# Kernel optimization log

Measured on AMD Instinct MI355X. Metric: run time of the kernel, lower is better.

## Reference

```python
import jax, jax.numpy as jnp
import numpy as np

N_NODES = 100000

def _mean_aggregate(h, edge_index, num_nodes):
    # PyG convention: edge_index[0]=source j, edge_index[1]=target i; mean over in-neighbors
    src, dst = edge_index[0], edge_index[1]
    summed = jax.ops.segment_sum(h[src], dst, num_segments=num_nodes)  # [N, D]
    cnt = jax.ops.segment_sum(jnp.ones((src.shape[0],), h.dtype), dst, num_segments=num_nodes)
    return summed / jnp.maximum(cnt, 1.0)[:, None]

def _sage_conv(h, edge_index, Wl, bl, Wr, num_nodes):
    agg = _mean_aggregate(h, edge_index, num_nodes)
    return agg @ Wl.T + bl + h @ Wr.T

def setup_inputs() -> dict:
    key = jax.random.key(0)
    ks = jax.random.split(key, 12)
    D = 64
    scale = 1.0 / np.sqrt(D)
    x = jax.random.normal(ks[0], (N_NODES, D), jnp.float32)
    edge_index = jax.random.randint(ks[1], (2, 1000000), 0, N_NODES, jnp.int32)
    edge_label_index = jax.random.randint(ks[2], (2, 200000), 0, N_NODES, jnp.int32)
    def w(k):
        return (jax.random.normal(k, (D, D), jnp.float32) * scale)
    return {
        'x': x,
        'edge_index': edge_index,
        'edge_label_index': edge_label_index,
        'W_lin': w(ks[3]), 'b_lin': jnp.zeros((D,), jnp.float32),
        'Wl1': w(ks[4]), 'bl1': jnp.zeros((D,), jnp.float32), 'Wr1': w(ks[5]),
        'Wl2': w(ks[6]), 'bl2': jnp.zeros((D,), jnp.float32), 'Wr2': w(ks[7]),
    }

def reference(x, edge_index, edge_label_index, W_lin, b_lin, Wl1, bl1, Wr1, Wl2, bl2, Wr2):
    h = x @ W_lin.T + b_lin                                   # node_lin
    h = jax.nn.relu(_sage_conv(h, edge_index, Wl1, bl1, Wr1, N_NODES))  # conv1 + relu
    h = _sage_conv(h, edge_index, Wl2, bl2, Wr2, N_NODES)               # conv2
    # edge dot-product classifier
    preds = jnp.sum(h[edge_label_index[0]] * h[edge_label_index[1]], axis=-1)  # [E_label]
    return preds
```

## Files before the change

### kernel.cpp

```cpp
#include <hip/hip_runtime.h>

#define DD 64
#define BW 256
#define NBMAX 512
#define CAPB 4096
#define CHUNK 8192
#define FILLPAD 16

typedef unsigned short u16;
typedef unsigned char u8;
typedef u16 ushort8v __attribute__((ext_vector_type(8)));
typedef short s16x8 __attribute__((ext_vector_type(8)));
typedef float f32x4 __attribute__((ext_vector_type(4)));
typedef float f32x2 __attribute__((ext_vector_type(2)));

__device__ __forceinline__ float bf2f(u16 u) {
    union { unsigned u32; float f; } x; x.u32 = (unsigned)u << 16; return x.f;
}
__device__ __forceinline__ u16 f2bf(float f) {
    union { float f; unsigned u; } x; x.f = f;
    unsigned r = (x.u + 0x7fffu + ((x.u >> 16) & 1u)) >> 16;
    return (u16)r;
}

__device__ __forceinline__ uint4 pack16_fp8(ushort8v s0, ushort8v s1) {
    uint4 pk;
    int w;
    w = __builtin_amdgcn_cvt_pk_fp8_f32(bf2f(s0[0]), bf2f(s0[1]), 0, false);
    w = __builtin_amdgcn_cvt_pk_fp8_f32(bf2f(s0[2]), bf2f(s0[3]), w, true);
    pk.x = (unsigned)w;
    w = __builtin_amdgcn_cvt_pk_fp8_f32(bf2f(s0[4]), bf2f(s0[5]), 0, false);
    w = __builtin_amdgcn_cvt_pk_fp8_f32(bf2f(s0[6]), bf2f(s0[7]), w, true);
    pk.y = (unsigned)w;
    w = __builtin_amdgcn_cvt_pk_fp8_f32(bf2f(s1[0]), bf2f(s1[1]), 0, false);
    w = __builtin_amdgcn_cvt_pk_fp8_f32(bf2f(s1[2]), bf2f(s1[3]), w, true);
    pk.z = (unsigned)w;
    w = __builtin_amdgcn_cvt_pk_fp8_f32(bf2f(s1[4]), bf2f(s1[5]), 0, false);
    w = __builtin_amdgcn_cvt_pk_fp8_f32(bf2f(s1[6]), bf2f(s1[7]), w, true);
    pk.w = (unsigned)w;
    return pk;
}

#define ACC16(u) do { \
    f32x2 _p; \
    _p = __builtin_amdgcn_cvt_pk_f32_fp8((int)(u).x, false); a[0]  += _p[0]; a[1]  += _p[1]; \
    _p = __builtin_amdgcn_cvt_pk_f32_fp8((int)(u).x, true);  a[2]  += _p[0]; a[3]  += _p[1]; \
    _p = __builtin_amdgcn_cvt_pk_f32_fp8((int)(u).y, false); a[4]  += _p[0]; a[5]  += _p[1]; \
    _p = __builtin_amdgcn_cvt_pk_f32_fp8((int)(u).y, true);  a[6]  += _p[0]; a[7]  += _p[1]; \
    _p = __builtin_amdgcn_cvt_pk_f32_fp8((int)(u).z, false); a[8]  += _p[0]; a[9]  += _p[1]; \
    _p = __builtin_amdgcn_cvt_pk_f32_fp8((int)(u).z, true);  a[10] += _p[0]; a[11] += _p[1]; \
    _p = __builtin_amdgcn_cvt_pk_f32_fp8((int)(u).w, false); a[12] += _p[0]; a[13] += _p[1]; \
    _p = __builtin_amdgcn_cvt_pk_f32_fp8((int)(u).w, true);  a[14] += _p[0]; a[15] += _p[1]; \
} while (0)

__global__ __launch_bounds__(256) void k_partlin(
    const int* __restrict__ ei, int n_edges, int nb_chunk,
    int* __restrict__ fill, unsigned* __restrict__ part,
    const float* __restrict__ w1, const float* __restrict__ w2,
    const float* __restrict__ w3, const float* __restrict__ w4,
    u16* __restrict__ wb,
    const float* __restrict__ A, const float* __restrict__ W,
    const float* __restrict__ bias, u16* __restrict__ out, u8* __restrict__ out8,
    int n_nodes) {
    __shared__ int hist[NBMAX];
    __shared__ int curs[NBMAX];
    __shared__ u16 stage[64 * DD];
    int t = threadIdx.x;
    if ((int)blockIdx.x < nb_chunk) {
        {
            int i = blockIdx.x * 256 + t;
            if (i < 4 * DD * DD) {
                int mat = i >> 12, off = i & 4095;
                const float* src = (mat == 0) ? w1 : (mat == 1) ? w2 : (mat == 2) ? w3 : w4;
                wb[DD * DD + i] = f2bf(src[off]);
            }
        }
        hist[t] = 0; hist[256 + t] = 0;
        __syncthreads();
        int c0 = blockIdx.x * CHUNK;
        int c1 = min(n_edges, c0 + CHUNK);
        int nloc = c1 - c0;
        int nvec = ((n_edges & 3) == 0) ? (nloc & ~3) : 0;
        for (int e4 = t * 4; e4 < nvec; e4 += 1024) {
            int4 d4 = *(const int4*)(ei + n_edges + c0 + e4);
            atomicAdd(&hist[d4.x >> 8], 1);
            atomicAdd(&hist[d4.y >> 8], 1);
            atomicAdd(&hist[d4.z >> 8], 1);
            atomicAdd(&hist[d4.w >> 8], 1);
        }
        for (int e = nvec + t; e < nloc; e += 256)
            atomicAdd(&hist[ei[n_edges + c0 + e] >> 8], 1);
        __syncthreads();
        #pragma unroll
        for (int k = 0; k < 2; ++k) {
            int idx = k * 256 + t;
            int h = hist[idx];
            int base = 0;
            if (h > 0) base = atomicAdd(&fill[idx * FILLPAD], h);
            curs[idx] = base;
        }
        __syncthreads();
        for (int e4 = t * 4; e4 < nvec; e4 += 1024) {
            int4 d4 = *(const int4*)(ei + n_edges + c0 + e4);
            int4 s4 = *(const int4*)(ei + c0 + e4);
            {
                int b = d4.x >> 8; int pos = atomicAdd(&curs[b], 1);
                if (pos < CAPB) part[(size_t)b * CAPB + pos] = ((unsigned)s4.x << 8) | (unsigned)(d4.x & 255);
            }
            {
                int b = d4.y >> 8; int pos = atomicAdd(&curs[b], 1);
                if (pos < CAPB) part[(size_t)b * CAPB + pos] = ((unsigned)s4.y << 8) | (unsigned)(d4.y & 255);
            }
            {
                int b = d4.z >> 8; int pos = atomicAdd(&curs[b], 1);
                if (pos < CAPB) part[(size_t)b * CAPB + pos] = ((unsigned)s4.z << 8) | (unsigned)(d4.z & 255);
            }
            {
                int b = d4.w >> 8; int pos = atomicAdd(&curs[b], 1);
                if (pos < CAPB) part[(size_t)b * CAPB + pos] = ((unsigned)s4.w << 8) | (unsigned)(d4.w & 255);
            }
        }
        for (int e = nvec + t; e < nloc; e += 256) {
            int dst = ei[n_edges + c0 + e];
            int src = ei[c0 + e];
            int b = dst >> 8;
            int pos = atomicAdd(&curs[b], 1);
            if (pos < CAPB)
                part[(size_t)b * CAPB + pos] = ((unsigned)src << 8) | (unsigned)(dst & 255);
        }
    } else {
        int bid = (int)blockIdx.x - nb_chunk;
        int w = t >> 6;
        int lane = t & 63;
        int col = lane & 15;
        int quad = lane >> 4;
        int m0 = bid * 64 + w * 16;
        int arow = m0 + col;
        if (arow > n_nodes - 1) arow = n_nodes - 1;

        f32x4 acc[4];
        #pragma unroll
        for (int nt = 0; nt < 4; ++nt) {
            float bv = bias[nt * 16 + col];
            acc[nt] = (f32x4){bv, bv, bv, bv};
        }
        #pragma unroll
        for (int ks = 0; ks < 2; ++ks) {
            int k0 = ks * 32 + quad * 8;
            const float* p = A + (size_t)arow * DD + k0;
            float4 v0 = *(const float4*)p;
            float4 v1 = *(const float4*)(p + 4);
            s16x8 a;
            a[0] = (short)f2bf(v0.x); a[1] = (short)f2bf(v0.y);
            a[2] = (short)f2bf(v0.z); a[3] = (short)f2bf(v0.w);
            a[4] = (short)f2bf(v1.x); a[5] = (short)f2bf(v1.y);
            a[6] = (short)f2bf(v1.z); a[7] = (short)f2bf(v1.w);
            #pragma unroll
            for (int nt = 0; nt < 4; ++nt) {
                const float* wp = W + (size_t)(nt * 16 + col) * DD + k0;
                float4 b0 = *(const float4*)wp;
                float4 b1 = *(const float4*)(wp + 4);
                s16x8 bfr;
                bfr[0] = (short)f2bf(b0.x); bfr[1] = (short)f2bf(b0.y);
                bfr[2] = (short)f2bf(b0.z); bfr[3] = (short)f2bf(b0.w);
                bfr[4] = (short)f2bf(b1.x); bfr[5] = (short)f2bf(b1.y);
                bfr[6] = (short)f2bf(b1.z); bfr[7] = (short)f2bf(b1.w);
                acc[nt] = __builtin_amdgcn_mfma_f32_16x16x32_bf16(a, bfr, acc[nt], 0, 0, 0);
            }
        }
        #pragma unroll
        for (int nt = 0; nt < 4; ++nt)
            #pragma unroll
            for (int i = 0; i < 4; ++i) {
                int rloc = w * 16 + quad * 4 + i;
                int dsw = (nt * 16 + col) ^ ((rloc & 3) << 4);
                stage[rloc * DD + dsw] = f2bf(acc[nt][i]);
            }
        __threadfence_block();
        {
            int rr = w * 16 + (lane >> 2);
            int sg = lane & 3;
            int m = bid * 64 + rr;
            if (m < n_nodes) {
                int se = (sg ^ (rr & 3)) * 16;
                ushort8v s0 = *(ushort8v*)(stage + rr * DD + se);
                ushort8v s1 = *(ushort8v*)(stage + rr * DD + se + 8);
                *(ushort8v*)(out + (size_t)m * DD + sg * 16) = s0;
                *(ushort8v*)(out + (size_t)m * DD + sg * 16 + 8) = s1;
                *(uint4*)(out8 + (size_t)m * DD + sg * 16) = pack16_fp8(s0, s1);
            }
        }
    }
}

__global__ __launch_bounds__(256) void k_build(const unsigned* __restrict__ part,
                        const int* __restrict__ fill,
                        int* __restrict__ row_start, int* __restrict__ row_deg,
                        int* __restrict__ csr, int n_nodes) {
    __shared__ int cnt_l[BW];
    __shared__ int sc[BW];
    __shared__ unsigned csr_l[CAPB];
    int t = threadIdx.x;
    int b = blockIdx.x;
    int beg = b * CAPB;
    int size = min(fill[b * FILLPAD], CAPB);

    cnt_l[t] = 0;
    __syncthreads();
    for (int j = t; j < size; j += 256)
        atomicAdd(&cnt_l[part[beg + j] & 255], 1);
    __syncthreads();
    int v0 = cnt_l[t];
    sc[t] = v0;
    cnt_l[t] = 0;
    __syncthreads();
    for (int off = 1; off < 256; off <<= 1) {
        int a = (t >= off) ? sc[t - off] : 0;
        __syncthreads();
        if (t >= off) sc[t] += a;
        __syncthreads();
    }
    {
        int n0 = b * BW + t;
        if (n0 < n_nodes) {
            row_start[n0] = beg + ((t == 0) ? 0 : sc[t - 1]);
            row_deg[n0] = v0;
        }
    }
    for (int j = t; j < size; j += 256) {
        unsigned p = part[beg + j];
        int dl = (int)(p & 255u);
        int pos = ((dl == 0) ? 0 : sc[dl - 1]) + atomicAdd(&cnt_l[dl], 1);
        csr_l[pos] = p >> 8;
    }
    __syncthreads();
    for (int i = t; i < size; i += 256) csr[beg + i] = (int)csr_l[i];
}

__global__ __launch_bounds__(256) void k_conv(
    const u16* __restrict__ h, const u8* __restrict__ h8,
    const int* __restrict__ row_start, const int* __restrict__ row_deg,
    const int* __restrict__ csr,
    const u16* __restrict__ Wl, const u16* __restrict__ Wr,
    const float* __restrict__ bias, u16* __restrict__ out, u8* __restrict__ out8,
    int n_nodes, int relu) {
    __shared__ u16 mean_l[64 * DD];
    int t = threadIdx.x;
    int w = t >> 6, lane = t & 63;
    int nn = lane >> 2;
    int r = lane & 3;
    int m0 = blockIdx.x * 64;

    {
        int li = w * 16 + nn;
        int n = m0 + li;
        int beg = 0, end = 0;
        if (n < n_nodes) { beg = row_start[n]; end = beg + row_deg[n]; }
        float a[16];
        #pragma unroll
        for (int kk = 0; kk < 16; ++kk) a[kk] = 0.f;
        int j = beg;
        for (; j + 3 < end; j += 4) {
            int s0 = csr[j], s1 = csr[j + 1], s2 = csr[j + 2], s3 = csr[j + 3];
            uint4 u0 = *(const uint4*)(h8 + (size_t)s0 * DD + r * 16);
            uint4 u1 = *(const uint4*)(h8 + (size_t)s1 * DD + r * 16);
            uint4 u2 = *(const uint4*)(h8 + (size_t)s2 * DD + r * 16);
            uint4 u3 = *(const uint4*)(h8 + (size_t)s3 * DD + r * 16);
            ACC16(u0); ACC16(u1); ACC16(u2); ACC16(u3);
        }
        for (; j < end; ++j) {
            uint4 u0 = *(const uint4*)(h8 + (size_t)csr[j] * DD + r * 16);
            ACC16(u0);
        }
        int deg = end - beg;
        float inv = (deg > 0) ? 1.0f / (float)deg : 0.0f;
        ushort8v o0, o1;
        #pragma unroll
        for (int kk = 0; kk < 8; ++kk) { o0[kk] = f2bf(a[kk] * inv); o1[kk] = f2bf(a[8 + kk] * inv); }
        *(ushort8v*)(mean_l + li * DD + r * 16) = o0;
        *(ushort8v*)(mean_l + li * DD + r * 16 + 8) = o1;
    }
    __threadfence_block();

    int col = lane & 15;
    int quad = lane >> 4;
    int arow = m0 + w * 16 + col;
    if (arow > n_nodes - 1) arow = n_nodes - 1;

    f32x4 acc[4];
    #pragma unroll
    for (int nt = 0; nt < 4; ++nt) {
        float bv = bias[nt * 16 + col];
        acc[nt] = (f32x4){bv, bv, bv, bv};
    }
    #pragma unroll
    for (int ks = 0; ks < 2; ++ks) {
        int k0 = ks * 32 + quad * 8;
        s16x8 am = *(const s16x8*)(mean_l + (w * 16 + col) * DD + k0);
        s16x8 ah = *(const s16x8*)(h + (size_t)arow * DD + k0);
        #pragma unroll
        for (int nt = 0; nt < 4; ++nt) {
            s16x8 bl = *(const s16x8*)(Wl + (nt * 16 + col) * DD + k0);
            acc[nt] = __builtin_amdgcn_mfma_f32_16x16x32_bf16(am, bl, acc[nt], 0, 0, 0);
            s16x8 br = *(const s16x8*)(Wr + (nt * 16 + col) * DD + k0);
            acc[nt] = __builtin_amdgcn_mfma_f32_16x16x32_bf16(ah, br, acc[nt], 0, 0, 0);
        }
    }
    #pragma unroll
    for (int nt = 0; nt < 4; ++nt)
        #pragma unroll
        for (int i = 0; i < 4; ++i) {
            float v = acc[nt][i];
            if (relu) v = fmaxf(v, 0.f);
            int rloc = w * 16 + quad * 4 + i;
            int dsw = (nt * 16 + col) ^ ((rloc & 3) << 4);
            mean_l[rloc * DD + dsw] = f2bf(v);
        }
    __threadfence_block();
    {
        int rr = w * 16 + (lane >> 2);
        int sg = lane & 3;
        int m = m0 + rr;
        if (m < n_nodes) {
            int se = (sg ^ (rr & 3)) * 16;
            ushort8v s0 = *(ushort8v*)(mean_l + rr * DD + se);
            ushort8v s1 = *(ushort8v*)(mean_l + rr * DD + se + 8);
            *(ushort8v*)(out + (size_t)m * DD + sg * 16) = s0;
            *(ushort8v*)(out + (size_t)m * DD + sg * 16 + 8) = s1;
            if (out8)
                *(uint4*)(out8 + (size_t)m * DD + sg * 16) = pack16_fp8(s0, s1);
        }
    }
}

__global__ void k_pred(const u16* __restrict__ h, const int* __restrict__ eli,
                       int n_label, float* __restrict__ out) {
    int t = threadIdx.x;
    int e = blockIdx.x * 16 + (t >> 4);
    if (e >= n_label) return;
    int g = (t >> 3) & 1;
    int r = t & 7;
    int node = g ? eli[n_label + e] : eli[e];
    ushort8v v = *(const ushort8v*)(h + (size_t)node * DD + r * 8);
    float s = 0.f;
    #pragma unroll
    for (int kk = 0; kk < 8; ++kk) {
        float f = bf2f(v[kk]);
        s += f * __shfl_xor(f, 8, 64);
    }
    #pragma unroll
    for (int off = 1; off < 8; off <<= 1) s += __shfl_xor(s, off, 64);
    if ((t & 15) == 0) out[e] = s;
}

extern "C" void kernel_launch(void* const* d_in, const int* in_sizes, int n_in,
                              void* d_out, int out_size, void* d_ws, size_t ws_size,
                              hipStream_t stream) {
    const float* x     = (const float*)d_in[0];
    const int*   ei    = (const int*)d_in[1];
    const int*   eli   = (const int*)d_in[2];
    const float* W_lin = (const float*)d_in[3];
    const float* b_lin = (const float*)d_in[4];
    const float* Wl1   = (const float*)d_in[5];
    const float* bl1   = (const float*)d_in[6];
    const float* Wr1   = (const float*)d_in[7];
    const float* Wl2   = (const float*)d_in[8];
    const float* bl2   = (const float*)d_in[9];
    const float* Wr2   = (const float*)d_in[10];

    int n_nodes = in_sizes[0] / DD;
    int n_edges = in_sizes[1] / 2;
    int n_label = in_sizes[2] / 2;
    float* out = (float*)d_out;

    int nb = (n_nodes + BW - 1) / BW;

    char* ws = (char*)d_ws;
    size_t hbytes = (size_t)n_nodes * DD * sizeof(u16);
    u16* hA   = (u16*)ws; ws += hbytes;
    u16* hB   = (u16*)ws; ws += hbytes;
    u8* h8A   = (u8*)ws;  ws += (size_t)n_nodes * DD;
    u8* h8B   = (u8*)ws;  ws += (size_t)n_nodes * DD;
    int* row_start = (int*)ws; ws += (size_t)((n_nodes + 3) & ~3) * sizeof(int);
    int* row_deg   = (int*)ws; ws += (size_t)((n_nodes + 3) & ~3) * sizeof(int);
    int* fill      = (int*)ws; ws += (size_t)NBMAX * FILLPAD * sizeof(int);
    u16* wb        = (u16*)ws; ws += 5 * DD * DD * sizeof(u16);
    unsigned* part = (unsigned*)ws; ws += (size_t)nb * CAPB * sizeof(unsigned);
    int* csr       = (int*)ws; ws += (size_t)nb * CAPB * sizeof(int);

    int nb_chunk = (n_edges + CHUNK - 1) / CHUNK;
    int nb_gemm = (n_nodes + 63) / 64;
    int nb_pred = (n_label + 15) / 16;

    (void)hipMemsetAsync(fill, 0, (size_t)NBMAX * FILLPAD * sizeof(int), stream);
    k_partlin<<<nb_chunk + nb_gemm, 256, 0, stream>>>(
        ei, n_edges, nb_chunk, fill, part,
        Wl1, Wr1, Wl2, Wr2, wb,
        x, W_lin, b_lin, hA, h8A, n_nodes);

    k_build<<<nb, 256, 0, stream>>>(part, fill, row_start, row_deg, csr, n_nodes);

    k_conv<<<nb_gemm, 256, 0, stream>>>(hA, h8A, row_start, row_deg, csr,
                                        wb + 4096, wb + 2 * 4096, bl1, hB, h8B, n_nodes, 1);

    k_conv<<<nb_gemm, 256, 0, stream>>>(hB, h8B, row_start, row_deg, csr,
                                        wb + 3 * 4096, wb + 4 * 4096, bl2, hA, nullptr, n_nodes, 0);

    k_pred<<<nb_pred, 256, 0, stream>>>(hA, eli, n_label, out);
}
```

Baseline: 198.4 us.

## Fuse CSR build into first conv kernel using per-quarter shared-memory buckets

Removes the separate k_build kernel. The first conv launch now has each 64-node block scan its 256-node partition bucket, build a local CSR in shared memory, and aggregate neighbours from it directly. The block also writes row_start, row_deg and csr for the second conv. CHUNK is halved to change the partition kernel's grid. Each partition bucket is now read four times, once per quarter block, and neighbour lists are capped at QCAP per quarter, which could silently drop edges if a quarter overflows.

```diff
diff --git a/kernel.cpp b/kernel.cpp
--- a/kernel.cpp
+++ b/kernel.cpp
@@ -4,7 +4,8 @@
 #define BW 256
 #define NBMAX 512
 #define CAPB 4096
-#define CHUNK 8192
+#define QCAP 1024
+#define CHUNK 4096
 #define FILLPAD 16
 
 typedef unsigned short u16;
@@ -193,86 +194,108 @@
     }
 }
 
-__global__ __launch_bounds__(256) void k_build(const unsigned* __restrict__ part,
-                        const int* __restrict__ fill,
-                        int* __restrict__ row_start, int* __restrict__ row_deg,
-                        int* __restrict__ csr, int n_nodes) {
-    __shared__ int cnt_l[BW];
-    __shared__ int sc[BW];
-    __shared__ unsigned csr_l[CAPB];
-    int t = threadIdx.x;
-    int b = blockIdx.x;
-    int beg = b * CAPB;
-    int size = min(fill[b * FILLPAD], CAPB);
-
-    cnt_l[t] = 0;
-    __syncthreads();
-    for (int j = t; j < size; j += 256)
-        atomicAdd(&cnt_l[part[beg + j] & 255], 1);
-    __syncthreads();
-    int v0 = cnt_l[t];
-    sc[t] = v0;
-    cnt_l[t] = 0;
-    __syncthreads();
-    for (int off = 1; off < 256; off <<= 1) {
-        int a = (t >= off) ? sc[t - off] : 0;
-        __syncthreads();
-        if (t >= off) sc[t] += a;
-        __syncthreads();
-    }
-    {
-        int n0 = b * BW + t;
-        if (n0 < n_nodes) {
-            row_start[n0] = beg + ((t == 0) ? 0 : sc[t - 1]);
-            row_deg[n0] = v0;
-        }
-    }
-    for (int j = t; j < size; j += 256) {
-        unsigned p = part[beg + j];
-        int dl = (int)(p & 255u);
-        int pos = ((dl == 0) ? 0 : sc[dl - 1]) + atomicAdd(&cnt_l[dl], 1);
-        csr_l[pos] = p >> 8;
-    }
-    __syncthreads();
-    for (int i = t; i < size; i += 256) csr[beg + i] = (int)csr_l[i];
-}
-
 __global__ __launch_bounds__(256) void k_conv(
     const u16* __restrict__ h, const u8* __restrict__ h8,
-    const int* __restrict__ row_start, const int* __restrict__ row_deg,
-    const int* __restrict__ csr,
+    const unsigned* __restrict__ part, const int* __restrict__ fill,
+    int* __restrict__ row_start, int* __restrict__ row_deg, int* __restrict__ csr,
     const u16* __restrict__ Wl, const u16* __restrict__ Wr,
     const float* __restrict__ bias, u16* __restrict__ out, u8* __restrict__ out8,
-    int n_nodes, int relu) {
+    int n_nodes, int relu, int build) {
     __shared__ u16 mean_l[64 * DD];
+    __shared__ int csr_l[QCAP];
+    __shared__ int hist64[64];
+    __shared__ int cnt64[64];
+    __shared__ int scan64[65];
     int t = threadIdx.x;
     int w = t >> 6, lane = t & 63;
-    int nn = lane >> 2;
-    int r = lane & 3;
     int m0 = blockIdx.x * 64;
 
+    if (build) {
+        int b = m0 >> 8;
+        int q = (m0 >> 6) & 3;
+        int qlo = q << 6;
+        int pbeg = b * CAPB;
+        int size = min(fill[b * FILLPAD], CAPB);
+        if (t < 64) { hist64[t] = 0; cnt64[t] = 0; }
+        __syncthreads();
+        for (int j = t; j < size; j += 256) {
+            int dl = (int)(part[pbeg + j] & 255u) - qlo;
+            if ((unsigned)dl < 64u) atomicAdd(&hist64[dl], 1);
+        }
+        __syncthreads();
+        if (t < 64) {
+            int s = hist64[t];
+            #pragma unroll
+            for (int off = 1; off < 64; off <<= 1) {
+                int u = __shfl_up(s, off, 64);
+                if (t >= off) s += u;
+            }
+            scan64[t + 1] = s;
+            if (t == 0) scan64[0] = 0;
+        }
+        __syncthreads();
+        for (int j = t; j < size; j += 256) {
+            unsigned p = part[pbeg + j];
+            int dl = (int)(p & 255u) - qlo;
+            if ((unsigned)dl < 64u) {
+                int pos = scan64[dl] + atomicAdd(&cnt64[dl], 1);
+                if (pos < QCAP) csr_l[pos] = (int)(p >> 8);
+            }
+        }
+        __syncthreads();
+        int qbase = (b * 4 + q) * QCAP;
+        if (t < 64) {
+            int n = m0 + t;
+            if (n < n_nodes) { row_start[n] = qbase + scan64[t]; row_deg[n] = hist64[t]; }
+        }
+        int tot = min(scan64[64], QCAP);
+        for (int i = t; i < tot; i += 256) csr[qbase + i] = csr_l[i];
+    }
+
     {
+        int nn = lane >> 2;
+        int r = lane & 3;
         int li = w * 16 + nn;
         int n = m0 + li;
-        int beg = 0, end = 0;
-        if (n < n_nodes) { beg = row_start[n]; end = beg + row_deg[n]; }
         float a[16];
         #pragma unroll
         for (int kk = 0; kk < 16; ++kk) a[kk] = 0.f;
-        int j = beg;
-        for (; j + 3 < end; j += 4) {
-            int s0 = csr[j], s1 = csr[j + 1], s2 = csr[j + 2], s3 = csr[j + 3];
-            uint4 u0 = *(const uint4*)(h8 + (size_t)s0 * DD + r * 16);
-            uint4 u1 = *(const uint4*)(h8 + (size_t)s1 * DD + r * 16);
-            uint4 u2 = *(const uint4*)(h8 + (size_t)s2 * DD + r * 16);
-            uint4 u3 = *(const uint4*)(h8 + (size_t)s3 * DD + r * 16);
-            ACC16(u0); ACC16(u1); ACC16(u2); ACC16(u3);
-        }
-        for (; j < end; ++j) {
-            uint4 u0 = *(const uint4*)(h8 + (size_t)csr[j] * DD + r * 16);
-            ACC16(u0);
-        }
-        int deg = end - beg;
+        int deg;
+        if (build) {
+            int beg = scan64[li];
+            int end = min(beg + hist64[li], QCAP);
+            deg = end - beg;
+            int j = beg;
+            for (; j + 3 < end; j += 4) {
+                int s0 = csr_l[j], s1 = csr_l[j + 1], s2 = csr_l[j + 2], s3 = csr_l[j + 3];
+                uint4 u0 = *(const uint4*)(h8 + (size_t)s0 * DD + r * 16);
+                uint4 u1 = *(const uint4*)(h8 + (size_t)s1 * DD + r * 16);
+                uint4 u2 = *(const uint4*)(h8 + (size_t)s2 * DD + r * 16);
+                uint4 u3 = *(const uint4*)(h8 + (size_t)s3 * DD + r * 16);
+                ACC16(u0); ACC16(u1); ACC16(u2); ACC16(u3);
+            }
+            for (; j < end; ++j) {
+                uint4 u0 = *(const uint4*)(h8 + (size_t)csr_l[j] * DD + r * 16);
+                ACC16(u0);
+            }
+        } else {
+            int beg = 0, end = 0;
+            if (n < n_nodes) { beg = row_start[n]; end = beg + row_deg[n]; }
+            deg = end - beg;
+            int j = beg;
+            for (; j + 3 < end; j += 4) {
+                int s0 = csr[j], s1 = csr[j + 1], s2 = csr[j + 2], s3 = csr[j + 3];
+                uint4 u0 = *(const uint4*)(h8 + (size_t)s0 * DD + r * 16);
+                uint4 u1 = *(const uint4*)(h8 + (size_t)s1 * DD + r * 16);
+                uint4 u2 = *(const uint4*)(h8 + (size_t)s2 * DD + r * 16);
+                uint4 u3 = *(const uint4*)(h8 + (size_t)s3 * DD + r * 16);
+                ACC16(u0); ACC16(u1); ACC16(u2); ACC16(u3);
+            }
+            for (; j < end; ++j) {
+                uint4 u0 = *(const uint4*)(h8 + (size_t)csr[j] * DD + r * 16);
+                ACC16(u0);
+            }
+        }
         float inv = (deg > 0) ? 1.0f / (float)deg : 0.0f;
         ushort8v o0, o1;
         #pragma unroll
@@ -398,13 +421,13 @@
         Wl1, Wr1, Wl2, Wr2, wb,
         x, W_lin, b_lin, hA, h8A, n_nodes);
 
-    k_build<<<nb, 256, 0, stream>>>(part, fill, row_start, row_deg, csr, n_nodes);
-
-    k_conv<<<nb_gemm, 256, 0, stream>>>(hA, h8A, row_start, row_deg, csr,
-                                        wb + 4096, wb + 2 * 4096, bl1, hB, h8B, n_nodes, 1);
-
-    k_conv<<<nb_gemm, 256, 0, stream>>>(hB, h8B, row_start, row_deg, csr,
-                                        wb + 3 * 4096, wb + 4 * 4096, bl2, hA, nullptr, n_nodes, 0);
+    k_conv<<<nb_gemm, 256, 0, stream>>>(hA, h8A, part, fill,
+                                        row_start, row_deg, csr,
+                                        wb + 4096, wb + 2 * 4096, bl1, hB, h8B, n_nodes, 1, 1);
+
+    k_conv<<<nb_gemm, 256, 0, stream>>>(hB, h8B, part, fill,
+                                        row_start, row_deg, csr,
+                                        wb + 3 * 4096, wb + 4 * 4096, bl2, hA, nullptr, n_nodes, 0, 0);
 
     k_pred<<<nb_pred, 256, 0, stream>>>(hA, eli, n_label, out);
 }
```

New measurement: 200.1 us. No clear change (+0.8%).

## Stage CSR span in LDS and unroll gather by 12 with zero-row padding

Applied to the files above, without the earlier changes.

k_conv now loads the block's contiguous CSR neighbor range into shared memory, then gathers 12 fp8 neighbor rows per iteration. Out-of-range slots point at a zeroed pad row, so there is no scalar tail loop and more loads are in flight. If the span exceeds the cap, it falls back to the global-CSR path. Separately, the partition chunk size is halved and k_pred handles 4 label edges per thread-group iteration with fewer blocks. These changes add LDS use and a block barrier, which may lower occupancy.

```diff
diff --git a/kernel.cpp b/kernel.cpp
--- a/kernel.cpp
+++ b/kernel.cpp
@@ -4,8 +4,9 @@
 #define BW 256
 #define NBMAX 512
 #define CAPB 4096
-#define CHUNK 8192
+#define CHUNK 4096
 #define FILLPAD 16
+#define SPAN_CAP 3072
 
 typedef unsigned short u16;
 typedef unsigned char u8;
@@ -240,39 +241,76 @@
 __global__ __launch_bounds__(256) void k_conv(
     const u16* __restrict__ h, const u8* __restrict__ h8,
     const int* __restrict__ row_start, const int* __restrict__ row_deg,
-    const int* __restrict__ csr,
+    const int* __restrict__ csr, const u8* __restrict__ zrow,
     const u16* __restrict__ Wl, const u16* __restrict__ Wr,
     const float* __restrict__ bias, u16* __restrict__ out, u8* __restrict__ out8,
     int n_nodes, int relu) {
     __shared__ u16 mean_l[64 * DD];
+    __shared__ int csr_s[SPAN_CAP + 12];
     int t = threadIdx.x;
     int w = t >> 6, lane = t & 63;
-    int nn = lane >> 2;
-    int r = lane & 3;
     int m0 = blockIdx.x * 64;
 
+    int nlast = min(m0 + 63, n_nodes - 1);
+    int sbeg = row_start[m0];
+    int span = row_start[nlast] + row_deg[nlast] - sbeg;
+    bool lds_ok = (span <= SPAN_CAP);
+    if (lds_ok) {
+        for (int i = t; i < span; i += 256) csr_s[i] = csr[sbeg + i];
+        if (t < 12) csr_s[span + t] = 0;
+        __syncthreads();
+    }
+
     {
+        int nn = lane >> 2;
+        int r = lane & 3;
         int li = w * 16 + nn;
         int n = m0 + li;
         int beg = 0, end = 0;
         if (n < n_nodes) { beg = row_start[n]; end = beg + row_deg[n]; }
+        int deg = end - beg;
         float a[16];
         #pragma unroll
         for (int kk = 0; kk < 16; ++kk) a[kk] = 0.f;
-        int j = beg;
-        for (; j + 3 < end; j += 4) {
-            int s0 = csr[j], s1 = csr[j + 1], s2 = csr[j + 2], s3 = csr[j + 3];
-            uint4 u0 = *(const uint4*)(h8 + (size_t)s0 * DD + r * 16);
-            uint4 u1 = *(const uint4*)(h8 + (size_t)s1 * DD + r * 16);
-            uint4 u2 = *(const uint4*)(h8 + (size_t)s2 * DD + r * 16);
-            uint4 u3 = *(const uint4*)(h8 + (size_t)s3 * DD + r * 16);
-            ACC16(u0); ACC16(u1); ACC16(u2); ACC16(u3);
-        }
-        for (; j < end; ++j) {
-            uint4 u0 = *(const uint4*)(h8 + (size_t)csr[j] * DD + r * 16);
-            ACC16(u0);
-        }
-        int deg = end - beg;
+        if (lds_ok) {
+            int je = end - sbeg;
+            size_t roff = (size_t)(r * 16);
+            for (int jj = beg - sbeg; jj < je; jj += 12) {
+                int cnt = je - jj;
+                #define GP(k) const u8* p##k = (k < cnt) ? (h8 + (size_t)csr_s[jj + k] * DD) : zrow;
+                GP(0) GP(1) GP(2) GP(3) GP(4) GP(5) GP(6) GP(7) GP(8) GP(9) GP(10) GP(11)
+                #undef GP
+                uint4 u0  = *(const uint4*)(p0  + roff);
+                uint4 u1  = *(const uint4*)(p1  + roff);
+                uint4 u2  = *(const uint4*)(p2  + roff);
+                uint4 u3  = *(const uint4*)(p3  + roff);
+                uint4 u4  = *(const uint4*)(p4  + roff);
+                uint4 u5  = *(const uint4*)(p5  + roff);
+                uint4 u6  = *(const uint4*)(p6  + roff);
+                uint4 u7  = *(const uint4*)(p7  + roff);
+                uint4 u8_ = *(const uint4*)(p8  + roff);
+                uint4 u9  = *(const uint4*)(p9  + roff);
+                uint4 u10 = *(const uint4*)(p10 + roff);
+                uint4 u11 = *(const uint4*)(p11 + roff);
+                ACC16(u0);  ACC16(u1);  ACC16(u2);  ACC16(u3);
+                ACC16(u4);  ACC16(u5);  ACC16(u6);  ACC16(u7);
+                ACC16(u8_); ACC16(u9);  ACC16(u10); ACC16(u11);
+            }
+        } else {
+            int j = beg;
+            for (; j + 3 < end; j += 4) {
+                int s0 = csr[j], s1 = csr[j + 1], s2 = csr[j + 2], s3 = csr[j + 3];
+                uint4 u0 = *(const uint4*)(h8 + (size_t)s0 * DD + r * 16);
+                uint4 u1 = *(const uint4*)(h8 + (size_t)s1 * DD + r * 16);
+                uint4 u2 = *(const uint4*)(h8 + (size_t)s2 * DD + r * 16);
+                uint4 u3 = *(const uint4*)(h8 + (size_t)s3 * DD + r * 16);
+                ACC16(u0); ACC16(u1); ACC16(u2); ACC16(u3);
+            }
+            for (; j < end; ++j) {
+                uint4 u0 = *(const uint4*)(h8 + (size_t)csr[j] * DD + r * 16);
+                ACC16(u0);
+            }
+        }
         float inv = (deg > 0) ? 1.0f / (float)deg : 0.0f;
         ushort8v o0, o1;
         #pragma unroll
@@ -336,21 +374,25 @@
 __global__ void k_pred(const u16* __restrict__ h, const int* __restrict__ eli,
                        int n_label, float* __restrict__ out) {
     int t = threadIdx.x;
-    int e = blockIdx.x * 16 + (t >> 4);
-    if (e >= n_label) return;
     int g = (t >> 3) & 1;
     int r = t & 7;
-    int node = g ? eli[n_label + e] : eli[e];
-    ushort8v v = *(const ushort8v*)(h + (size_t)node * DD + r * 8);
-    float s = 0.f;
     #pragma unroll
-    for (int kk = 0; kk < 8; ++kk) {
-        float f = bf2f(v[kk]);
-        s += f * __shfl_xor(f, 8, 64);
-    }
-    #pragma unroll
-    for (int off = 1; off < 8; off <<= 1) s += __shfl_xor(s, off, 64);
-    if ((t & 15) == 0) out[e] = s;
+    for (int it = 0; it < 4; ++it) {
+        int e = blockIdx.x * 64 + it * 16 + (t >> 4);
+        if (e < n_label) {
+            int node = g ? eli[n_label + e] : eli[e];
+            ushort8v v = *(const ushort8v*)(h + (size_t)node * DD + r * 8);
+            float s = 0.f;
+            #pragma unroll
+            for (int kk = 0; kk < 8; ++kk) {
+                float f = bf2f(v[kk]);
+                s += f * __shfl_xor(f, 8, 64);
+            }
+            #pragma unroll
+            for (int off = 1; off < 8; off <<= 1) s += __shfl_xor(s, off, 64);
+            if ((t & 15) == 0) out[e] = s;
+        }
+    }
 }
 
 extern "C" void kernel_launch(void* const* d_in, const int* in_sizes, int n_in,
@@ -384,15 +426,16 @@
     int* row_start = (int*)ws; ws += (size_t)((n_nodes + 3) & ~3) * sizeof(int);
     int* row_deg   = (int*)ws; ws += (size_t)((n_nodes + 3) & ~3) * sizeof(int);
     int* fill      = (int*)ws; ws += (size_t)NBMAX * FILLPAD * sizeof(int);
+    u8* zrow       = (u8*)ws; ws += 64;
     u16* wb        = (u16*)ws; ws += 5 * DD * DD * sizeof(u16);
     unsigned* part = (unsigned*)ws; ws += (size_t)nb * CAPB * sizeof(unsigned);
     int* csr       = (int*)ws; ws += (size_t)nb * CAPB * sizeof(int);
 
     int nb_chunk = (n_edges + CHUNK - 1) / CHUNK;
     int nb_gemm = (n_nodes + 63) / 64;
-    int nb_pred = (n_label + 15) / 16;
-
-    (void)hipMemsetAsync(fill, 0, (size_t)NBMAX * FILLPAD * sizeof(int), stream);
+    int nb_pred = (n_label + 63) / 64;
+
+    (void)hipMemsetAsync(fill, 0, (size_t)NBMAX * FILLPAD * sizeof(int) + 64, stream);
     k_partlin<<<nb_chunk + nb_gemm, 256, 0, stream>>>(
         ei, n_edges, nb_chunk, fill, part,
         Wl1, Wr1, Wl2, Wr2, wb,
@@ -400,10 +443,10 @@
 
     k_build<<<nb, 256, 0, stream>>>(part, fill, row_start, row_deg, csr, n_nodes);
 
-    k_conv<<<nb_gemm, 256, 0, stream>>>(hA, h8A, row_start, row_deg, csr,
+    k_conv<<<nb_gemm, 256, 0, stream>>>(hA, h8A, row_start, row_deg, csr, zrow,
                                         wb + 4096, wb + 2 * 4096, bl1, hB, h8B, n_nodes, 1);
 
-    k_conv<<<nb_gemm, 256, 0, stream>>>(hB, h8B, row_start, row_deg, csr,
+    k_conv<<<nb_gemm, 256, 0, stream>>>(hB, h8B, row_start, row_deg, csr, zrow,
                                         wb + 3 * 4096, wb + 4 * 4096, bl2, hA, nullptr, n_nodes, 0);
 
     k_pred<<<nb_pred, 256, 0, stream>>>(hA, eli, n_label, out);
```

Measured after the change: 211.4 us. 1.07x slower.
